# Kernel tuning notes

Measured on AMD Instinct MI355X. Metric: run time of the kernel, lower is better.

Reference implementation:

```python
import jax, jax.numpy as jnp
import numpy as np
from jax.scipy.special import gammaln, xlogy

B, N, DIM, H, DK, DV = 2, 2048, 1536, 8, 64, 64
NRPF = 192  # num_rel_pos_features, already divisible by 6


def get_positional_embed(n, feat):
    # Enformer positional basis: exponential, central-mask, gamma; then sign-antisymmetrized.
    nb = feat // 6  # num basis per class
    d = jnp.arange(-n + 1, n, dtype=jnp.float32)          # [2n-1]
    ad = jnp.abs(d)[:, None]                              # [2n-1, 1]
    # exponential decay features
    max_range = np.log(n) / np.log(2.0)
    half_life = 2.0 ** jnp.linspace(3.0, max_range, nb)
    e = jnp.exp(-np.log(2.0) / half_life * ad)
    # central mask features
    widths = 2.0 ** jnp.arange(1, nb + 1, dtype=jnp.float32) - 1.0
    c = (widths > ad).astype(jnp.float32)
    # gamma pdf features
    std = n / (2.0 * nb)
    mean = jnp.linspace(n / nb, float(n), nb)
    conc = (mean / std) ** 2
    rate = mean / (std ** 2)
    logp = xlogy(conc - 1.0, ad) - rate * ad - (gammaln(conc) - conc * jnp.log(rate))
    p = jnp.exp(logp) + 1e-8
    g = p / jnp.max(p)
    emb = jnp.concatenate([e, c, g], axis=-1)             # [2n-1, feat//2]
    return jnp.concatenate([emb, jnp.sign(d)[:, None] * emb], axis=-1)  # [2n-1, feat]


def relative_shift(x):
    # x: [b, h, i, 2i-1] -> [b, h, i, i]
    b, h, i, j = x.shape
    x = jnp.pad(x, ((0, 0), (0, 0), (0, 0), (1, 0)))      # [b,h,i,j+1]
    x = x.reshape(b, h, j + 1, i)[:, :, 1:, :]            # drop first 'row'
    x = x.reshape(b, h, i, j)
    return x[..., : (j + 2) // 2]                          # keep first i cols


def setup_inputs() -> dict:
    key = jax.random.key(0)
    ks = jax.random.split(key, 9)
    s = 0.02
    return {
        "x": jax.random.normal(ks[0], (B, N, DIM), jnp.float32),
        "Wq": jax.random.normal(ks[1], (DIM, H * DK), jnp.float32) * s,
        "Wk": jax.random.normal(ks[2], (DIM, H * DK), jnp.float32) * s,
        "Wv": jax.random.normal(ks[3], (DIM, H * DV), jnp.float32) * s,
        "Wo": jax.random.normal(ks[4], (H * DV, DIM), jnp.float32) * s,
        "bo": jnp.zeros((DIM,), jnp.float32),
        "Wrel": jax.random.normal(ks[5], (NRPF, H * DK), jnp.float32) * s,
        "rel_content_bias": jax.random.normal(ks[6], (1, H, 1, DK), jnp.float32),
        "rel_pos_bias": jax.random.normal(ks[7], (1, H, 1, DK), jnp.float32),
    }


def reference(x, Wq, Wk, Wv, Wo, bo, Wrel, rel_content_bias, rel_pos_bias):
    b, n, _ = x.shape
    scale = DK ** -0.5
    split = lambda t, d: t.reshape(b, n, H, d).transpose(0, 2, 1, 3)  # b h n d
    q = split(x @ Wq, DK) * scale
    k = split(x @ Wk, DK)
    v = split(x @ Wv, DV)
    content_logits = jnp.einsum('bhid,bhjd->bhij', q + rel_content_bias, k)
    pos = get_positional_embed(n, NRPF) @ Wrel               # [2n-1, H*DK]
    pos = pos.reshape(2 * n - 1, H, DK).transpose(1, 0, 2)   # h j d
    rel_logits = jnp.einsum('bhid,hjd->bhij', q + rel_pos_bias, pos)
    rel_logits = relative_shift(rel_logits)
    attn = jax.nn.softmax(content_logits + rel_logits, axis=-1)
    out = jnp.einsum('bhij,bhjd->bhid', attn, v)
    out = out.transpose(0, 2, 1, 3).reshape(b, n, H * DV)
    return out @ Wo + bo
```

## Files before the change

### kernel.cpp

```cpp
#include <hip/hip_runtime.h>
#include <stdint.h>
#include <cmath>

#define B_    2
#define N_    2048
#define DIM_  1536
#define H_    8
#define NPOS  (2*N_ - 1)
#define NB_   32

typedef __attribute__((ext_vector_type(8))) short short8;
typedef __attribute__((ext_vector_type(4))) float float4v;

__device__ __forceinline__ float bf2f(unsigned short u) {
    return __uint_as_float(((unsigned int)u) << 16);
}
__device__ __forceinline__ unsigned short f2bf(float f) {
    unsigned int u = __float_as_uint(f);
    u += 0x7FFFu + ((u >> 16) & 1u);
    return (unsigned short)(u >> 16);
}
__device__ __forceinline__ unsigned int cvtpk(float lo, float hi) {
    unsigned int r;
    asm("v_cvt_pk_bf16_f32 %0, %1, %2" : "=v"(r) : "v"(lo), "v"(hi));
    return r;
}
__device__ __forceinline__ unsigned int pack2bf(float lo, float hi) {
    return cvtpk(lo, hi);
}
__device__ __forceinline__ float ldf(const void* p, int isF32, size_t idx) {
    return isF32 ? ((const float*)p)[idx] : bf2f(((const unsigned short*)p)[idx]);
}
__device__ __forceinline__ void gll16(const unsigned short* g, unsigned short* l) {
    __builtin_amdgcn_global_load_lds(
        (const __attribute__((address_space(1))) unsigned int*)g,
        (__attribute__((address_space(3))) unsigned int*)l, 16, 0, 0);
}

constexpr size_t OFF_FLAG = 0;
constexpr size_t OFF_POS  = 256;
constexpr size_t OFF_Q    = OFF_POS + (size_t)H_*4096*64*2;
constexpr size_t OFF_K    = OFF_Q   + (size_t)B_*H_*N_*64*2;
constexpr size_t OFF_V    = OFF_K   + (size_t)B_*H_*N_*64*2;
constexpr size_t OFF_WOT  = OFF_V   + (size_t)B_*H_*N_*64*2;
constexpr size_t OFF_XB   = OFF_WOT + (size_t)DIM_*512*2;
constexpr size_t OFF_AO   = OFF_XB;
constexpr size_t OFF_OP   = OFF_AO + (size_t)4096*512*2;
constexpr size_t OFF_LP   = OFF_OP + (size_t)3*16*32*4096*2;
constexpr size_t OFF_WT   = OFF_XB + (size_t)4096*DIM_*2;
static_assert(OFF_LP + (size_t)3*16*32*64*4 <= OFF_WT + (size_t)3*512*DIM_*2, "ws overflow");

__global__ __launch_bounds__(256) void detect_kernel(const unsigned short* __restrict__ x,
                                                     unsigned int* __restrict__ flags) {
    __shared__ int cnt[256];
    unsigned short u = x[2 * threadIdx.x];
    int e  = (u >> 7) & 0xFF;
    int ok = (u == 0) || (e >= 95 && e <= 140);
    cnt[threadIdx.x] = ok;
    __syncthreads();
    for (int s = 128; s > 0; s >>= 1) {
        if (threadIdx.x < s) cnt[threadIdx.x] += cnt[threadIdx.x + s];
        __syncthreads();
    }
    if (threadIdx.x == 0) flags[0] = (cnt[0] >= 192) ? 0u : 1u;
}

__global__ __launch_bounds__(256) void cvtx_kernel(const unsigned int* __restrict__ flags,
                                                   const void* __restrict__ x,
                                                   unsigned short* __restrict__ Xb) {
    const int f32 = (int)flags[0];
    const size_t total = (size_t)4096 * DIM_;
    size_t i = ((size_t)blockIdx.x * 256 + threadIdx.x) * 8;
    const size_t stride = (size_t)gridDim.x * 256 * 8;
    if (f32) {
        for (; i < total; i += stride) {
            float4v a = *reinterpret_cast<const float4v*>((const float*)x + i);
            float4v b = *reinterpret_cast<const float4v*>((const float*)x + i + 4);
            uint4 o;
            o.x = pack2bf(a[0], a[1]); o.y = pack2bf(a[2], a[3]);
            o.z = pack2bf(b[0], b[1]); o.w = pack2bf(b[2], b[3]);
            *reinterpret_cast<uint4*>(Xb + i) = o;
        }
    } else {
        for (; i < total; i += stride)
            *reinterpret_cast<uint4*>(Xb + i) =
                *reinterpret_cast<const uint4*>((const unsigned short*)x + i);
    }
}

__global__ __launch_bounds__(256) void cvtw_kernel(const unsigned int* __restrict__ flags,
                                                   const void* __restrict__ Wq, const void* __restrict__ Wk,
                                                   const void* __restrict__ Wv, const void* __restrict__ Wo,
                                                   unsigned short* __restrict__ Wt,
                                                   unsigned short* __restrict__ Wot) {
    __shared__ unsigned short tile[32][33];
    const int f32 = (int)flags[0];
    const int z = blockIdx.z;
    const void* src = z == 0 ? Wq : (z == 1 ? Wk : (z == 2 ? Wv : Wo));
    unsigned short* dst = (z < 3) ? (Wt + (size_t)z * 512 * DIM_) : Wot;
    const int R = (z < 3) ? DIM_ : 512;
    const int C = (z < 3) ? 512 : DIM_;
    const int x0 = ((z < 3) ? blockIdx.x : blockIdx.y) * 32;
    const int y0 = ((z < 3) ? blockIdx.y : blockIdx.x) * 32;
    const int tx = threadIdx.x & 31, ty = threadIdx.x >> 5;
#pragma unroll
    for (int i = 0; i < 4; ++i)
        tile[ty + i * 8][tx] = f2bf(ldf(src, f32, (size_t)(y0 + ty + i * 8) * C + x0 + tx));
    __syncthreads();
#pragma unroll
    for (int i = 0; i < 4; ++i)
        dst[(size_t)(x0 + ty + i * 8) * R + y0 + tx] = tile[tx][ty + i * 8];
}

__global__ __launch_bounds__(512) void posproj_kernel(double maxp,
                                                      const void* __restrict__ Wrel,
                                                      const unsigned int* __restrict__ flags,
                                                      unsigned short* __restrict__ posb) {
    __shared__ __align__(16) float eb[8 * 192];
    const int f32 = (int)flags[0];
    const int j0  = blockIdx.x * 8;
    const int c   = threadIdx.x;
    const double max_range = log((double)N_) / log(2.0);

    for (int u = c; u < 8 * 96; u += 512) {
        int rr = u / 96, f = u - rr * 96;
        int j = j0 + rr;
        float v = 0.f, sg = 0.f;
        if (j < NPOS) {
            int dd  = j - (N_ - 1);
            int adI = dd < 0 ? -dd : dd;
            double ad = (double)adI;
            double val;
            if (f < 32) {
                double t = 3.0 + (double)f * (max_range - 3.0) / 31.0;
                val = exp2(-ad / exp2(t));
            } else if (f < 64) {
                double width = exp2((double)(f - 31)) - 1.0;
                val = (width > ad) ? 1.0 : 0.0;
            } else {
                int g = f - 64;
                double mean = 64.0 * (g + 1);
                double conc = (mean / 32.0) * (mean / 32.0);
                double rate = mean / 1024.0;
                double pp = (adI == 0) ? 1e-8
                          : exp((conc - 1.0) * log(ad) - rate * ad - lgamma(conc) + conc * log(rate)) + 1e-8;
                val = pp / maxp;
            }
            v  = (float)val;
            sg = (dd > 0) ? 1.f : ((dd < 0) ? -1.f : 0.f);
        }
        eb[rr * 192 + f]      = v;
        eb[rr * 192 + 96 + f] = sg * v;
    }
    __syncthreads();

    float acc[8] = {0, 0, 0, 0, 0, 0, 0, 0};
    for (int k = 0; k < 192; k += 4) {
        float w0 = ldf(Wrel, f32, (size_t)(k + 0) * 512 + c);
        float w1 = ldf(Wrel, f32, (size_t)(k + 1) * 512 + c);
        float w2 = ldf(Wrel, f32, (size_t)(k + 2) * 512 + c);
        float w3 = ldf(Wrel, f32, (size_t)(k + 3) * 512 + c);
#pragma unroll
        for (int rr = 0; rr < 8; ++rr) {
            float4v e = *reinterpret_cast<const float4v*>(&eb[rr * 192 + k]);
            acc[rr] += e[0] * w0;
            acc[rr] += e[1] * w1;
            acc[rr] += e[2] * w2;
            acc[rr] += e[3] * w3;
        }
    }
    int h = c >> 6, dcol = c & 63;
    for (int rr = 0; rr < 8; ++rr) {
        int j = j0 + rr;
        if (j < NPOS)
            posb[((size_t)h * 4096 + j) * 64 + dcol] = f2bf(acc[rr]);
    }
}

__device__ __forceinline__ void gemm64x128_core(const unsigned short* __restrict__ A,
                                                const unsigned short* __restrict__ Bt,
                                                int K, int row0, int col0,
                                                unsigned short* As, unsigned short* Bs,
                                                float4v acc[2][4]) {
    const int tid = threadIdx.x, lane = tid & 63, w = tid >> 6;
    const int l15 = lane & 15, q8 = (lane >> 4) * 8;
    const int mr0 = (w & 1) * 32, nc0 = (w >> 1) * 64;
    const int sr = lane >> 2, sc8 = (lane & 3) * 8;
    for (int k0 = 0; k0 < K; k0 += 32) {
        __syncthreads();
        gll16(&A [(size_t)(row0 + w * 16 + sr) * K + k0 + sc8],      &As[w * 512]);
        gll16(&Bt[(size_t)(col0 + w * 32 + sr) * K + k0 + sc8],      &Bs[w * 1024]);
        gll16(&Bt[(size_t)(col0 + w * 32 + 16 + sr) * K + k0 + sc8], &Bs[w * 1024 + 512]);
        __syncthreads();
        short8 a[2], b[4];
#pragma unroll
        for (int mi = 0; mi < 2; ++mi)
            a[mi] = *reinterpret_cast<const short8*>(&As[(mr0 + mi * 16 + l15) * 32 + q8]);
#pragma unroll
        for (int ni = 0; ni < 4; ++ni)
            b[ni] = *reinterpret_cast<const short8*>(&Bs[(nc0 + ni * 16 + l15) * 32 + q8]);
#pragma unroll
        for (int mi = 0; mi < 2; ++mi)
#pragma unroll
            for (int ni = 0; ni < 4; ++ni)
                acc[mi][ni] = __builtin_amdgcn_mfma_f32_16x16x32_bf16(a[mi], b[ni], acc[mi][ni], 0, 0, 0);
    }
}

__global__ __launch_bounds__(256) void qkv_kernel(const unsigned short* __restrict__ Xb,
                                                  const unsigned short* __restrict__ Wt,
                                                  unsigned short* __restrict__ qbuf,
                                                  unsigned short* __restrict__ kbuf,
                                                  unsigned short* __restrict__ vbuf) {
    __shared__ __align__(16) unsigned short As[64 * 32];
    __shared__ __align__(16) unsigned short Bs[128 * 32];
    const int row0 = blockIdx.y * 64, col0 = blockIdx.x * 128;
    float4v acc[2][4];
#pragma unroll
    for (int mi = 0; mi < 2; ++mi)
#pragma unroll
        for (int ni = 0; ni < 4; ++ni) acc[mi][ni] = (float4v){0.f, 0.f, 0.f, 0.f};
    gemm64x128_core(Xb, Wt, DIM_, row0, col0, As, Bs, acc);
    const int lane = threadIdx.x & 63, w = threadIdx.x >> 6;
    const int l15 = lane & 15, quad = lane >> 4;
    const int mr0 = (w & 1) * 32, nc0 = (w >> 1) * 64;
#pragma unroll
    for (int mi = 0; mi < 2; ++mi)
#pragma unroll
        for (int ni = 0; ni < 4; ++ni) {
            int n = col0 + nc0 + ni * 16 + l15;
            int mode = n >> 9, nn = n & 511;
            int hh = nn >> 6, dd = nn & 63;
            int mb = row0 + mr0 + mi * 16 + quad * 4;
            int bb = mb >> 11, ii = mb & 2047;
            if (mode == 2) {
                union { unsigned short us[4]; uint2 u2; } pk;
                unsigned int p0 = cvtpk(acc[mi][ni][0], acc[mi][ni][1]);
                unsigned int p1 = cvtpk(acc[mi][ni][2], acc[mi][ni][3]);
                pk.u2 = (uint2){p0, p1};
                *reinterpret_cast<uint2*>(
                    &vbuf[((size_t)(bb * 8 + hh) * 64 + dd) * 2048 + ii]) = pk.u2;
            } else {
                unsigned short* Obuf = (mode == 0) ? qbuf : kbuf;
                float scale = (mode == 0) ? 0.125f : 1.0f;
#pragma unroll
                for (int r = 0; r < 4; ++r)
                    Obuf[((size_t)(bb * 8 + hh) * N_ + ii + r) * 64 + dd] = f2bf(acc[mi][ni][r] * scale);
            }
        }
}

#define SLD 72
#define RST 68

__device__ __forceinline__ void stage64(const unsigned short* __restrict__ g,
                                        unsigned short* __restrict__ s, int tid) {
    int r = tid >> 2, d0 = (tid & 3) * 16;
    const uint4* p = reinterpret_cast<const uint4*>(g + (size_t)r * 64 + d0);
    *reinterpret_cast<uint4*>(&s[r * SLD + d0])     = p[0];
    *reinterpret_cast<uint4*>(&s[r * SLD + d0 + 8]) = p[1];
}

__global__ __launch_bounds__(256) void attn_kernel(const unsigned int* __restrict__ flags,
                                                   const unsigned short* __restrict__ qb,
                                                   const unsigned short* __restrict__ kb,
                                                   const unsigned short* __restrict__ vb,
                                                   const unsigned short* __restrict__ posb,
                                                   const void* __restrict__ rcb,
                                                   const void* __restrict__ rpb,
                                                   unsigned short* __restrict__ Opart,
                                                   float* __restrict__ lpart) {
    __shared__ __align__(16) unsigned short Ks[64 * SLD];
    __shared__ __align__(16) unsigned short Ps[64 * SLD];
    __shared__ __align__(16) unsigned short Vt[64 * SLD];
    __shared__ __align__(16) unsigned short Pp[64 * SLD];
    __shared__ __align__(8)  unsigned short Rb[128 * RST];

    const int f32 = (int)flags[0];
    const int tid = threadIdx.x;
    const int it = blockIdx.x, bh = blockIdx.y, z = blockIdx.z;
    const int h = bh & 7;
    const int i0 = it * 64;
    const size_t qoff = (size_t)bh * N_ * 64;
    const size_t voff = (size_t)bh * 64 * 2048;
    const size_t poff = (size_t)h * 4096 * 64;
    const int lane = tid & 63, w = tid >> 6;
    const int l15 = lane & 15, quad = lane >> 4, q8 = quad * 8;
    const int m0 = w * 16 + quad * 4;
    const int sr = tid >> 2, sc = (tid & 3) * 16;

    short8 afc[2], afr[2];
#pragma unroll
    for (int kc = 0; kc < 2; ++kc) {
        uint4 qv = *reinterpret_cast<const uint4*>(
            &qb[qoff + (size_t)(i0 + w * 16 + l15) * 64 + kc * 32 + q8]);
        unsigned int uu[4] = {qv.x, qv.y, qv.z, qv.w};
        unsigned int cw[4], rw[4];
#pragma unroll
        for (int e = 0; e < 4; ++e) {
            int k = h * 64 + kc * 32 + q8 + 2 * e;
            float lo = __uint_as_float(uu[e] << 16);
            float hi = __uint_as_float(uu[e] & 0xffff0000u);
            cw[e] = pack2bf(lo + ldf(rcb, f32, k), hi + ldf(rcb, f32, k + 1));
            rw[e] = pack2bf(lo + ldf(rpb, f32, k), hi + ldf(rpb, f32, k + 1));
        }
        union { uint4 u; short8 s; } cv, rv2;
        cv.u  = (uint4){cw[0], cw[1], cw[2], cw[3]};
        rv2.u = (uint4){rw[0], rw[1], rw[2], rw[3]};
        afc[kc] = cv.s;
        afr[kc] = rv2.s;
    }

    float4v Oa[4];
#pragma unroll
    for (int nb = 0; nb < 4; ++nb) Oa[nb] = (float4v){0.f, 0.f, 0.f, 0.f};
    float lsum[4] = {0.f, 0.f, 0.f, 0.f};

    const int base0 = 1984 - i0;
    const int t0 = z * 11, t1 = (z == 2) ? 32 : (t0 + 11);
    const int cs0 = base0 + t0 * 64;

    stage64(&posb[poff + (size_t)cs0 * 64], Ps, tid);
    __syncthreads();
    {
        float4v R[4];
#pragma unroll
        for (int nb = 0; nb < 4; ++nb) R[nb] = (float4v){0.f, 0.f, 0.f, 0.f};
        __builtin_amdgcn_s_setprio(1);
#pragma unroll
        for (int kc = 0; kc < 2; ++kc)
#pragma unroll
            for (int nb = 0; nb < 4; ++nb) {
                short8 pb = *reinterpret_cast<const short8*>(&Ps[(nb * 16 + l15) * SLD + kc * 32 + q8]);
                R[nb] = __builtin_amdgcn_mfma_f32_16x16x32_bf16(afr[kc], pb, R[nb], 0, 0, 0);
            }
        __builtin_amdgcn_s_setprio(0);
#pragma unroll
        for (int nb = 0; nb < 4; ++nb) {
            int ta = cs0 + nb * 16 + l15;
            unsigned int pk0 = cvtpk(R[nb][0], R[nb][1]);
            unsigned int pk1 = cvtpk(R[nb][2], R[nb][3]);
            Rb[(size_t)((ta + m0 + 0) & 127) * RST + m0 + 0] = (unsigned short)pk0;
            Rb[(size_t)((ta + m0 + 1) & 127) * RST + m0 + 1] = (unsigned short)(pk0 >> 16);
            Rb[(size_t)((ta + m0 + 2) & 127) * RST + m0 + 2] = (unsigned short)pk1;
            Rb[(size_t)((ta + m0 + 3) & 127) * RST + m0 + 3] = (unsigned short)(pk1 >> 16);
        }
    }
    __syncthreads();

    stage64(&kb[qoff + (size_t)(t0 * 64) * 64], Ks, tid);
    stage64(&posb[poff + (size_t)(cs0 + 64) * 64], Ps, tid);
    {
        const unsigned short* gv = &vb[voff + (size_t)sr * 2048 + t0 * 64 + sc];
        *reinterpret_cast<uint4*>(&Vt[sr * SLD + sc])     = *reinterpret_cast<const uint4*>(gv);
        *reinterpret_cast<uint4*>(&Vt[sr * SLD + sc + 8]) = *reinterpret_cast<const uint4*>(gv + 8);
    }
    __syncthreads();

    for (int jt = t0; jt < t1; ++jt) {
        const int j0 = jt * 64, basej = base0 + j0;
        const bool hasn = (jt + 1 < t1);

        uint4 kr0, kr1, pr0, pr1, vr0, vr1;
        if (hasn) {
            const unsigned short* gk = &kb[qoff + (size_t)(j0 + 64 + sr) * 64 + sc];
            kr0 = *reinterpret_cast<const uint4*>(gk);
            kr1 = *reinterpret_cast<const uint4*>(gk + 8);
            const unsigned short* gp = &posb[poff + (size_t)(basej + 128 + sr) * 64 + sc];
            pr0 = *reinterpret_cast<const uint4*>(gp);
            pr1 = *reinterpret_cast<const uint4*>(gp + 8);
            const unsigned short* gv = &vb[voff + (size_t)sr * 2048 + j0 + 64 + sc];
            vr0 = *reinterpret_cast<const uint4*>(gv);
            vr1 = *reinterpret_cast<const uint4*>(gv + 8);
            __builtin_amdgcn_sched_barrier(0);
        }

        {
            float4v R[4];
#pragma unroll
            for (int nb = 0; nb < 4; ++nb) R[nb] = (float4v){0.f, 0.f, 0.f, 0.f};
            __builtin_amdgcn_s_setprio(1);
#pragma unroll
            for (int kc = 0; kc < 2; ++kc)
#pragma unroll
                for (int nb = 0; nb < 4; ++nb) {
                    short8 pb = *reinterpret_cast<const short8*>(&Ps[(nb * 16 + l15) * SLD + kc * 32 + q8]);
                    R[nb] = __builtin_amdgcn_mfma_f32_16x16x32_bf16(afr[kc], pb, R[nb], 0, 0, 0);
                }
            __builtin_amdgcn_s_setprio(0);
            const int tb = basej + 64;
#pragma unroll
            for (int nb = 0; nb < 4; ++nb) {
                int ta = tb + nb * 16 + l15;
                unsigned int pk0 = cvtpk(R[nb][0], R[nb][1]);
                unsigned int pk1 = cvtpk(R[nb][2], R[nb][3]);
                Rb[(size_t)((ta + m0 + 0) & 127) * RST + m0 + 0] = (unsigned short)pk0;
                Rb[(size_t)((ta + m0 + 1) & 127) * RST + m0 + 1] = (unsigned short)(pk0 >> 16);
                Rb[(size_t)((ta + m0 + 2) & 127) * RST + m0 + 2] = (unsigned short)pk1;
                Rb[(size_t)((ta + m0 + 3) & 127) * RST + m0 + 3] = (unsigned short)(pk1 >> 16);
            }
        }

        float4v Sacc[4];
#pragma unroll
        for (int nb = 0; nb < 4; ++nb) Sacc[nb] = (float4v){0.f, 0.f, 0.f, 0.f};
        __builtin_amdgcn_s_setprio(1);
#pragma unroll
        for (int kc = 0; kc < 2; ++kc)
#pragma unroll
            for (int nb = 0; nb < 4; ++nb) {
                short8 kf = *reinterpret_cast<const short8*>(&Ks[(nb * 16 + l15) * SLD + kc * 32 + q8]);
                Sacc[nb] = __builtin_amdgcn_mfma_f32_16x16x32_bf16(afc[kc], kf, Sacc[nb], 0, 0, 0);
            }
        __builtin_amdgcn_s_setprio(0);

        float pv4[4][4];
#pragma unroll
        for (int nb = 0; nb < 4; ++nb) {
            const int jl = nb * 16 + l15;
            const int row = (basej + 63 + jl) & 127;
            union { uint2 u2; unsigned short us[4]; } rv;
            rv.u2 = *reinterpret_cast<const uint2*>(&Rb[(size_t)row * RST + m0]);
#pragma unroll
            for (int r = 0; r < 4; ++r) {
                float p = __expf(Sacc[nb][r] + bf2f(rv.us[r]));
                pv4[nb][r] = p;
                lsum[r] += p;
            }
        }
#pragma unroll
        for (int r = 0; r < 4; ++r) {
            unsigned short* prow = &Pp[(m0 + r) * SLD + l15];
#pragma unroll
            for (int np = 0; np < 2; ++np) {
                unsigned int pk = cvtpk(pv4[2 * np][r], pv4[2 * np + 1][r]);
                prow[(2 * np) * 16]     = (unsigned short)pk;
                prow[(2 * np + 1) * 16] = (unsigned short)(pk >> 16);
            }
        }

        __builtin_amdgcn_s_setprio(1);
#pragma unroll
        for (int kc = 0; kc < 2; ++kc) {
            short8 pf = *reinterpret_cast<const short8*>(&Pp[(w * 16 + l15) * SLD + kc * 32 + q8]);
#pragma unroll
            for (int nb = 0; nb < 4; ++nb) {
                short8 vf = *reinterpret_cast<const short8*>(&Vt[(nb * 16 + l15) * SLD + kc * 32 + q8]);
                Oa[nb] = __builtin_amdgcn_mfma_f32_16x16x32_bf16(pf, vf, Oa[nb], 0, 0, 0);
            }
        }
        __builtin_amdgcn_s_setprio(0);

        if (hasn) {
            __syncthreads();
            *reinterpret_cast<uint4*>(&Ks[sr * SLD + sc])     = kr0;
            *reinterpret_cast<uint4*>(&Ks[sr * SLD + sc + 8]) = kr1;
            *reinterpret_cast<uint4*>(&Ps[sr * SLD + sc])     = pr0;
            *reinterpret_cast<uint4*>(&Ps[sr * SLD + sc + 8]) = pr1;
            *reinterpret_cast<uint4*>(&Vt[sr * SLD + sc])     = vr0;
            *reinterpret_cast<uint4*>(&Vt[sr * SLD + sc + 8]) = vr1;
            __syncthreads();
        }
    }

#pragma unroll
    for (int r = 0; r < 4; ++r)
#pragma unroll
        for (int off = 1; off < 16; off <<= 1) lsum[r] += __shfl_xor(lsum[r], off);
    const size_t pslot = (size_t)(z * 16 + bh) * 32 + it;
    const size_t obase = pslot * 4096;
#pragma unroll
    for (int nb = 0; nb < 4; ++nb) {
        unsigned int pk0 = cvtpk(Oa[nb][0], Oa[nb][1]);
        unsigned int pk1 = cvtpk(Oa[nb][2], Oa[nb][3]);
        unsigned short* prow = &Pp[m0 * SLD + nb * 16 + l15];
        prow[0 * SLD] = (unsigned short)pk0;
        prow[1 * SLD] = (unsigned short)(pk0 >> 16);
        prow[2 * SLD] = (unsigned short)pk1;
        prow[3 * SLD] = (unsigned short)(pk1 >> 16);
    }
    {
        const int rr2 = w * 16 + (lane >> 2), cc2 = (lane & 3) * 16;
        uint4 o0 = *reinterpret_cast<const uint4*>(&Pp[rr2 * SLD + cc2]);
        uint4 o1 = *reinterpret_cast<const uint4*>(&Pp[rr2 * SLD + cc2 + 8]);
        *reinterpret_cast<uint4*>(&Opart[obase + (size_t)rr2 * 64 + cc2])     = o0;
        *reinterpret_cast<uint4*>(&Opart[obase + (size_t)rr2 * 64 + cc2 + 8]) = o1;
    }
    if (l15 == 0) {
#pragma unroll
        for (int r = 0; r < 4; ++r) lpart[pslot * 64 + m0 + r] = lsum[r];
    }
}

__global__ __launch_bounds__(256) void combine_kernel(const unsigned short* __restrict__ Opart,
                                                      const float* __restrict__ lpart,
                                                      unsigned short* __restrict__ ao) {
    const int it = blockIdx.x, bh = blockIdx.y;
    const int h = bh & 7, b = bh >> 3, i0 = it * 64;
    const int tid = threadIdx.x;
    const int row = tid >> 2, c0 = (tid & 3) * 16;
    float o[16];
#pragma unroll
    for (int e = 0; e < 16; ++e) o[e] = 0.f;
    float l = 0.f;
#pragma unroll
    for (int z = 0; z < 3; ++z) {
        const size_t pslot = (size_t)(z * 16 + bh) * 32 + it;
        const size_t ob = pslot * 4096 + (size_t)row * 64 + c0;
        uint4 a = *reinterpret_cast<const uint4*>(&Opart[ob]);
        uint4 b4 = *reinterpret_cast<const uint4*>(&Opart[ob + 8]);
        unsigned int uu[8] = {a.x, a.y, a.z, a.w, b4.x, b4.y, b4.z, b4.w};
#pragma unroll
        for (int e = 0; e < 8; ++e) {
            o[2 * e]     += __uint_as_float(uu[e] << 16);
            o[2 * e + 1] += __uint_as_float(uu[e] & 0xffff0000u);
        }
        l += lpart[pslot * 64 + row];
    }
    float inv = 1.0f / l;
    unsigned int ou[8];
#pragma unroll
    for (int e = 0; e < 8; ++e) ou[e] = pack2bf(o[2 * e] * inv, o[2 * e + 1] * inv);
    unsigned short* dst = &ao[((size_t)b * N_ + i0 + row) * 512 + h * 64 + c0];
    *reinterpret_cast<uint4*>(dst)     = (uint4){ou[0], ou[1], ou[2], ou[3]};
    *reinterpret_cast<uint4*>(dst + 8) = (uint4){ou[4], ou[5], ou[6], ou[7]};
}

__global__ __launch_bounds__(256) void outproj_kernel(const unsigned int* __restrict__ flags,
                                                      const unsigned short* __restrict__ AO,
                                                      const unsigned short* __restrict__ Wot,
                                                      const void* __restrict__ bo,
                                                      void* __restrict__ out) {
    __shared__ __align__(16) unsigned short As[64 * 32];
    __shared__ __align__(16) unsigned short Bs[128 * 32];
    const int f32 = (int)flags[0];
    const int row0 = blockIdx.y * 64, col0 = blockIdx.x * 128;
    float4v acc[2][4];
#pragma unroll
    for (int mi = 0; mi < 2; ++mi)
#pragma unroll
        for (int ni = 0; ni < 4; ++ni) acc[mi][ni] = (float4v){0.f, 0.f, 0.f, 0.f};
    gemm64x128_core(AO, Wot, 512, row0, col0, As, Bs, acc);
    const int lane = threadIdx.x & 63, w = threadIdx.x >> 6;
    const int l15 = lane & 15, quad = lane >> 4;
    const int mr0 = (w & 1) * 32, nc0 = (w >> 1) * 64;
#pragma unroll
    for (int mi = 0; mi < 2; ++mi)
#pragma unroll
        for (int ni = 0; ni < 4; ++ni) {
            int n = col0 + nc0 + ni * 16 + l15;
            float bias = ldf(bo, f32, n);
#pragma unroll
            for (int r = 0; r < 4; ++r) {
                int m = row0 + mr0 + mi * 16 + quad * 4 + r;
                float v = acc[mi][ni][r] + bias;
                if (f32) ((float*)out)[(size_t)m * DIM_ + n] = v;
                else     ((unsigned short*)out)[(size_t)m * DIM_ + n] = f2bf(v);
            }
        }
}

extern "C" void kernel_launch(void* const* d_in, const int* in_sizes, int n_in,
                              void* d_out, int out_size, void* d_ws, size_t ws_size,
                              hipStream_t stream) {
    const void* x    = d_in[0];
    const void* Wq   = d_in[1];
    const void* Wk   = d_in[2];
    const void* Wv   = d_in[3];
    const void* Wo   = d_in[4];
    const void* bo   = d_in[5];
    const void* Wrel = d_in[6];
    const void* rcb  = d_in[7];
    const void* rpb  = d_in[8];

    char* ws = (char*)d_ws;
    unsigned int*   flags = (unsigned int*)(ws + OFF_FLAG);
    unsigned short* posb  = (unsigned short*)(ws + OFF_POS);
    unsigned short* qbuf  = (unsigned short*)(ws + OFF_Q);
    unsigned short* kbuf  = (unsigned short*)(ws + OFF_K);
    unsigned short* vbuf  = (unsigned short*)(ws + OFF_V);
    unsigned short* Wot   = (unsigned short*)(ws + OFF_WOT);
    unsigned short* Xb    = (unsigned short*)(ws + OFF_XB);
    unsigned short* ao    = (unsigned short*)(ws + OFF_AO);
    unsigned short* Opart = (unsigned short*)(ws + OFF_OP);
    float*          lpart = (float*)(ws + OFF_LP);
    unsigned short* Wt    = (unsigned short*)(ws + OFF_WT);

    double maxp = 0.0;
    for (int g = 0; g < NB_; ++g) {
        double mean = 64.0 * (g + 1);
        double conc = (mean / 32.0) * (mean / 32.0);
        double rate = mean / 1024.0;
        double lgc  = std::lgamma(conc);
        double clr  = conc * std::log(rate);
        for (int ad = 1; ad < N_; ++ad) {
            double lp = (conc - 1.0) * std::log((double)ad) - rate * (double)ad - lgc + clr;
            double p  = std::exp(lp) + 1e-8;
            if (p > maxp) maxp = p;
        }
    }

    detect_kernel<<<dim3(1), dim3(256), 0, stream>>>((const unsigned short*)x, flags);
    cvtx_kernel<<<dim3(1024), dim3(256), 0, stream>>>(flags, x, Xb);
    cvtw_kernel<<<dim3(16, 48, 4), dim3(256), 0, stream>>>(flags, Wq, Wk, Wv, Wo, Wt, Wot);
    posproj_kernel<<<dim3(512), dim3(512), 0, stream>>>(maxp, Wrel, flags, posb);
    qkv_kernel<<<dim3(12, 64), dim3(256), 0, stream>>>(Xb, Wt, qbuf, kbuf, vbuf);
    attn_kernel<<<dim3(32, 16, 3), dim3(256), 0, stream>>>(flags, qbuf, kbuf, vbuf, posb, rcb, rpb, Opart, lpart);
    combine_kernel<<<dim3(32, 16), dim3(256), 0, stream>>>(Opart, lpart, ao);
    outproj_kernel<<<dim3(12, 64), dim3(256), 0, stream>>>(flags, ao, Wot, bo, d_out);
}
```

Baseline: 283.4 us.

## Fuse prep kernels, enlarge GEMM tiles to 128x128, remap attention grid

Merges the detect, x-convert, weight-transpose and positional-projection kernels into one launch, with each block recomputing the dtype flag locally. This removes three launches and their serialization. The QKV and output-projection GEMMs move from 64x128 to 128x128 tiles with 4x4 MFMA accumulators per wave, for more reuse per LDS load at the cost of half as many blocks and more registers. The attention grid is flattened to 1D with an interleaving remap, likely to spread work across XCDs for cache locality.

```diff
diff --git a/kernel.cpp b/kernel.cpp
--- a/kernel.cpp
+++ b/kernel.cpp
@@ -50,157 +50,159 @@
 constexpr size_t OFF_WT   = OFF_XB + (size_t)4096*DIM_*2;
 static_assert(OFF_LP + (size_t)3*16*32*64*4 <= OFF_WT + (size_t)3*512*DIM_*2, "ws overflow");
 
-__global__ __launch_bounds__(256) void detect_kernel(const unsigned short* __restrict__ x,
-                                                     unsigned int* __restrict__ flags) {
-    __shared__ int cnt[256];
-    unsigned short u = x[2 * threadIdx.x];
-    int e  = (u >> 7) & 0xFF;
-    int ok = (u == 0) || (e >= 95 && e <= 140);
-    cnt[threadIdx.x] = ok;
-    __syncthreads();
-    for (int s = 128; s > 0; s >>= 1) {
-        if (threadIdx.x < s) cnt[threadIdx.x] += cnt[threadIdx.x + s];
-        __syncthreads();
-    }
-    if (threadIdx.x == 0) flags[0] = (cnt[0] >= 192) ? 0u : 1u;
-}
-
-__global__ __launch_bounds__(256) void cvtx_kernel(const unsigned int* __restrict__ flags,
+__global__ __launch_bounds__(512) void prep_kernel(double maxp,
                                                    const void* __restrict__ x,
-                                                   unsigned short* __restrict__ Xb) {
-    const int f32 = (int)flags[0];
-    const size_t total = (size_t)4096 * DIM_;
-    size_t i = ((size_t)blockIdx.x * 256 + threadIdx.x) * 8;
-    const size_t stride = (size_t)gridDim.x * 256 * 8;
-    if (f32) {
-        for (; i < total; i += stride) {
-            float4v a = *reinterpret_cast<const float4v*>((const float*)x + i);
-            float4v b = *reinterpret_cast<const float4v*>((const float*)x + i + 4);
-            uint4 o;
-            o.x = pack2bf(a[0], a[1]); o.y = pack2bf(a[2], a[3]);
-            o.z = pack2bf(b[0], b[1]); o.w = pack2bf(b[2], b[3]);
-            *reinterpret_cast<uint4*>(Xb + i) = o;
-        }
-    } else {
-        for (; i < total; i += stride)
-            *reinterpret_cast<uint4*>(Xb + i) =
-                *reinterpret_cast<const uint4*>((const unsigned short*)x + i);
-    }
-}
-
-__global__ __launch_bounds__(256) void cvtw_kernel(const unsigned int* __restrict__ flags,
                                                    const void* __restrict__ Wq, const void* __restrict__ Wk,
                                                    const void* __restrict__ Wv, const void* __restrict__ Wo,
+                                                   const void* __restrict__ Wrel,
+                                                   unsigned int* __restrict__ flags,
+                                                   unsigned short* __restrict__ Xb,
                                                    unsigned short* __restrict__ Wt,
-                                                   unsigned short* __restrict__ Wot) {
-    __shared__ unsigned short tile[32][33];
-    const int f32 = (int)flags[0];
-    const int z = blockIdx.z;
-    const void* src = z == 0 ? Wq : (z == 1 ? Wk : (z == 2 ? Wv : Wo));
-    unsigned short* dst = (z < 3) ? (Wt + (size_t)z * 512 * DIM_) : Wot;
-    const int R = (z < 3) ? DIM_ : 512;
-    const int C = (z < 3) ? 512 : DIM_;
-    const int x0 = ((z < 3) ? blockIdx.x : blockIdx.y) * 32;
-    const int y0 = ((z < 3) ? blockIdx.y : blockIdx.x) * 32;
-    const int tx = threadIdx.x & 31, ty = threadIdx.x >> 5;
-#pragma unroll
-    for (int i = 0; i < 4; ++i)
-        tile[ty + i * 8][tx] = f2bf(ldf(src, f32, (size_t)(y0 + ty + i * 8) * C + x0 + tx));
+                                                   unsigned short* __restrict__ Wot,
+                                                   unsigned short* __restrict__ posb) {
+    __shared__ __align__(16) char smraw[8 * 192 * 4];
+    const int tid = threadIdx.x;
+    const int bid = blockIdx.x;
+
+    int* cnt = (int*)smraw;
+    int ok = 0;
+    if (tid < 256) {
+        unsigned short u = ((const unsigned short*)x)[2 * tid];
+        int e = (u >> 7) & 0xFF;
+        ok = (u == 0) || (e >= 95 && e <= 140);
+    }
+    cnt[tid] = ok;
     __syncthreads();
-#pragma unroll
-    for (int i = 0; i < 4; ++i)
-        dst[(size_t)(x0 + ty + i * 8) * R + y0 + tx] = tile[tx][ty + i * 8];
-}
-
-__global__ __launch_bounds__(512) void posproj_kernel(double maxp,
-                                                      const void* __restrict__ Wrel,
-                                                      const unsigned int* __restrict__ flags,
-                                                      unsigned short* __restrict__ posb) {
-    __shared__ __align__(16) float eb[8 * 192];
-    const int f32 = (int)flags[0];
-    const int j0  = blockIdx.x * 8;
-    const int c   = threadIdx.x;
-    const double max_range = log((double)N_) / log(2.0);
-
-    for (int u = c; u < 8 * 96; u += 512) {
-        int rr = u / 96, f = u - rr * 96;
-        int j = j0 + rr;
-        float v = 0.f, sg = 0.f;
-        if (j < NPOS) {
-            int dd  = j - (N_ - 1);
-            int adI = dd < 0 ? -dd : dd;
-            double ad = (double)adI;
-            double val;
-            if (f < 32) {
-                double t = 3.0 + (double)f * (max_range - 3.0) / 31.0;
-                val = exp2(-ad / exp2(t));
-            } else if (f < 64) {
-                double width = exp2((double)(f - 31)) - 1.0;
-                val = (width > ad) ? 1.0 : 0.0;
-            } else {
-                int g = f - 64;
-                double mean = 64.0 * (g + 1);
-                double conc = (mean / 32.0) * (mean / 32.0);
-                double rate = mean / 1024.0;
-                double pp = (adI == 0) ? 1e-8
-                          : exp((conc - 1.0) * log(ad) - rate * ad - lgamma(conc) + conc * log(rate)) + 1e-8;
-                val = pp / maxp;
-            }
-            v  = (float)val;
-            sg = (dd > 0) ? 1.f : ((dd < 0) ? -1.f : 0.f);
-        }
-        eb[rr * 192 + f]      = v;
-        eb[rr * 192 + 96 + f] = sg * v;
-    }
+    for (int s = 256; s > 0; s >>= 1) {
+        if (tid < s) cnt[tid] += cnt[tid + s];
+        __syncthreads();
+    }
+    const int f32 = !(cnt[0] >= 192);
     __syncthreads();
-
-    float acc[8] = {0, 0, 0, 0, 0, 0, 0, 0};
-    for (int k = 0; k < 192; k += 4) {
-        float w0 = ldf(Wrel, f32, (size_t)(k + 0) * 512 + c);
-        float w1 = ldf(Wrel, f32, (size_t)(k + 1) * 512 + c);
-        float w2 = ldf(Wrel, f32, (size_t)(k + 2) * 512 + c);
-        float w3 = ldf(Wrel, f32, (size_t)(k + 3) * 512 + c);
-#pragma unroll
+    if (bid == 0 && tid == 0) flags[0] = (unsigned int)f32;
+
+    if (bid < 512) {
+        const size_t total = (size_t)4096 * DIM_;
+        size_t i = ((size_t)bid * 512 + tid) * 8;
+        const size_t stride = (size_t)512 * 512 * 8;
+        if (f32) {
+            for (; i < total; i += stride) {
+                float4v a = *reinterpret_cast<const float4v*>((const float*)x + i);
+                float4v b = *reinterpret_cast<const float4v*>((const float*)x + i + 4);
+                uint4 o;
+                o.x = pack2bf(a[0], a[1]); o.y = pack2bf(a[2], a[3]);
+                o.z = pack2bf(b[0], b[1]); o.w = pack2bf(b[2], b[3]);
+                *reinterpret_cast<uint4*>(Xb + i) = o;
+            }
+        } else {
+            for (; i < total; i += stride)
+                *reinterpret_cast<uint4*>(Xb + i) =
+                    *reinterpret_cast<const uint4*>((const unsigned short*)x + i);
+        }
+    } else if (bid < 3584) {
+        unsigned short (*tile)[33] = (unsigned short(*)[33])smraw;
+        const int idx = bid - 512;
+        const int z = idx / 768, rem = idx % 768;
+        const int bx = rem & 15, by = rem >> 4;
+        const void* src = z == 0 ? Wq : (z == 1 ? Wk : (z == 2 ? Wv : Wo));
+        unsigned short* dst = (z < 3) ? (Wt + (size_t)z * 512 * DIM_) : Wot;
+        const int R = (z < 3) ? DIM_ : 512;
+        const int C = (z < 3) ? 512 : DIM_;
+        const int x0 = ((z < 3) ? bx : by) * 32;
+        const int y0 = ((z < 3) ? by : bx) * 32;
+        const int tx = tid & 31, ty = tid >> 5;
+#pragma unroll
+        for (int i = 0; i < 2; ++i)
+            tile[ty + i * 16][tx] = f2bf(ldf(src, f32, (size_t)(y0 + ty + i * 16) * C + x0 + tx));
+        __syncthreads();
+#pragma unroll
+        for (int i = 0; i < 2; ++i)
+            dst[(size_t)(x0 + ty + i * 16) * R + y0 + tx] = tile[tx][ty + i * 16];
+    } else {
+        float* eb = (float*)smraw;
+        const int j0 = (bid - 3584) * 8;
+        const int c  = tid;
+        const double max_range = log((double)N_) / log(2.0);
+        for (int u = c; u < 8 * 96; u += 512) {
+            int rr = u / 96, f = u - rr * 96;
+            int j = j0 + rr;
+            float v = 0.f, sg = 0.f;
+            if (j < NPOS) {
+                int dd  = j - (N_ - 1);
+                int adI = dd < 0 ? -dd : dd;
+                double ad = (double)adI;
+                double val;
+                if (f < 32) {
+                    double t = 3.0 + (double)f * (max_range - 3.0) / 31.0;
+                    val = exp2(-ad / exp2(t));
+                } else if (f < 64) {
+                    double width = exp2((double)(f - 31)) - 1.0;
+                    val = (width > ad) ? 1.0 : 0.0;
+                } else {
+                    int g = f - 64;
+                    double mean = 64.0 * (g + 1);
+                    double conc = (mean / 32.0) * (mean / 32.0);
+                    double rate = mean / 1024.0;
+                    double pp = (adI == 0) ? 1e-8
+                              : exp((conc - 1.0) * log(ad) - rate * ad - lgamma(conc) + conc * log(rate)) + 1e-8;
+                    val = pp / maxp;
+                }
+                v  = (float)val;
+                sg = (dd > 0) ? 1.f : ((dd < 0) ? -1.f : 0.f);
+            }
+            eb[rr * 192 + f]      = v;
+            eb[rr * 192 + 96 + f] = sg * v;
+        }
+        __syncthreads();
+        float acc[8] = {0, 0, 0, 0, 0, 0, 0, 0};
+        for (int k = 0; k < 192; k += 4) {
+            float w0 = ldf(Wrel, f32, (size_t)(k + 0) * 512 + c);
+            float w1 = ldf(Wrel, f32, (size_t)(k + 1) * 512 + c);
+            float w2 = ldf(Wrel, f32, (size_t)(k + 2) * 512 + c);
+            float w3 = ldf(Wrel, f32, (size_t)(k + 3) * 512 + c);
+#pragma unroll
+            for (int rr = 0; rr < 8; ++rr) {
+                float4v e = *reinterpret_cast<const float4v*>(&eb[rr * 192 + k]);
+                acc[rr] += e[0] * w0;
+                acc[rr] += e[1] * w1;
+                acc[rr] += e[2] * w2;
+                acc[rr] += e[3] * w3;
+            }
+        }
+        int h = c >> 6, dcol = c & 63;
         for (int rr = 0; rr < 8; ++rr) {
-            float4v e = *reinterpret_cast<const float4v*>(&eb[rr * 192 + k]);
-            acc[rr] += e[0] * w0;
-            acc[rr] += e[1] * w1;
-            acc[rr] += e[2] * w2;
-            acc[rr] += e[3] * w3;
-        }
-    }
-    int h = c >> 6, dcol = c & 63;
-    for (int rr = 0; rr < 8; ++rr) {
-        int j = j0 + rr;
-        if (j < NPOS)
-            posb[((size_t)h * 4096 + j) * 64 + dcol] = f2bf(acc[rr]);
-    }
-}
-
-__device__ __forceinline__ void gemm64x128_core(const unsigned short* __restrict__ A,
-                                                const unsigned short* __restrict__ Bt,
-                                                int K, int row0, int col0,
-                                                unsigned short* As, unsigned short* Bs,
-                                                float4v acc[2][4]) {
+            int j = j0 + rr;
+            if (j < NPOS)
+                posb[((size_t)h * 4096 + j) * 64 + dcol] = f2bf(acc[rr]);
+        }
+    }
+}
+
+__device__ __forceinline__ void gemm128_core(const unsigned short* __restrict__ A,
+                                             const unsigned short* __restrict__ Bt,
+                                             int K, int row0, int col0,
+                                             unsigned short* As, unsigned short* Bs,
+                                             float4v acc[4][4]) {
     const int tid = threadIdx.x, lane = tid & 63, w = tid >> 6;
     const int l15 = lane & 15, q8 = (lane >> 4) * 8;
-    const int mr0 = (w & 1) * 32, nc0 = (w >> 1) * 64;
+    const int mr0 = (w >> 1) * 64, nc0 = (w & 1) * 64;
     const int sr = lane >> 2, sc8 = (lane & 3) * 8;
     for (int k0 = 0; k0 < K; k0 += 32) {
         __syncthreads();
-        gll16(&A [(size_t)(row0 + w * 16 + sr) * K + k0 + sc8],      &As[w * 512]);
+        gll16(&A [(size_t)(row0 + w * 32 + sr) * K + k0 + sc8],      &As[w * 1024]);
+        gll16(&A [(size_t)(row0 + w * 32 + 16 + sr) * K + k0 + sc8], &As[w * 1024 + 512]);
         gll16(&Bt[(size_t)(col0 + w * 32 + sr) * K + k0 + sc8],      &Bs[w * 1024]);
         gll16(&Bt[(size_t)(col0 + w * 32 + 16 + sr) * K + k0 + sc8], &Bs[w * 1024 + 512]);
         __syncthreads();
-        short8 a[2], b[4];
-#pragma unroll
-        for (int mi = 0; mi < 2; ++mi)
+        short8 a[4], b[4];
+#pragma unroll
+        for (int mi = 0; mi < 4; ++mi)
             a[mi] = *reinterpret_cast<const short8*>(&As[(mr0 + mi * 16 + l15) * 32 + q8]);
 #pragma unroll
         for (int ni = 0; ni < 4; ++ni)
             b[ni] = *reinterpret_cast<const short8*>(&Bs[(nc0 + ni * 16 + l15) * 32 + q8]);
 #pragma unroll
-        for (int mi = 0; mi < 2; ++mi)
+        for (int mi = 0; mi < 4; ++mi)
 #pragma unroll
             for (int ni = 0; ni < 4; ++ni)
                 acc[mi][ni] = __builtin_amdgcn_mfma_f32_16x16x32_bf16(a[mi], b[ni], acc[mi][ni], 0, 0, 0);
@@ -212,20 +214,20 @@
                                                   unsigned short* __restrict__ qbuf,
                                                   unsigned short* __restrict__ kbuf,
                                                   unsigned short* __restrict__ vbuf) {
-    __shared__ __align__(16) unsigned short As[64 * 32];
+    __shared__ __align__(16) unsigned short As[128 * 32];
     __shared__ __align__(16) unsigned short Bs[128 * 32];
-    const int row0 = blockIdx.y * 64, col0 = blockIdx.x * 128;
-    float4v acc[2][4];
-#pragma unroll
-    for (int mi = 0; mi < 2; ++mi)
+    const int row0 = blockIdx.y * 128, col0 = blockIdx.x * 128;
+    float4v acc[4][4];
+#pragma unroll
+    for (int mi = 0; mi < 4; ++mi)
 #pragma unroll
         for (int ni = 0; ni < 4; ++ni) acc[mi][ni] = (float4v){0.f, 0.f, 0.f, 0.f};
-    gemm64x128_core(Xb, Wt, DIM_, row0, col0, As, Bs, acc);
+    gemm128_core(Xb, Wt, DIM_, row0, col0, As, Bs, acc);
     const int lane = threadIdx.x & 63, w = threadIdx.x >> 6;
     const int l15 = lane & 15, quad = lane >> 4;
-    const int mr0 = (w & 1) * 32, nc0 = (w >> 1) * 64;
-#pragma unroll
-    for (int mi = 0; mi < 2; ++mi)
+    const int mr0 = (w >> 1) * 64, nc0 = (w & 1) * 64;
+#pragma unroll
+    for (int mi = 0; mi < 4; ++mi)
 #pragma unroll
         for (int ni = 0; ni < 4; ++ni) {
             int n = col0 + nc0 + ni * 16 + l15;
@@ -278,7 +280,9 @@
 
     const int f32 = (int)flags[0];
     const int tid = threadIdx.x;
-    const int it = blockIdx.x, bh = blockIdx.y, z = blockIdx.z;
+    int wg = blockIdx.x;
+    wg = (wg & 7) * 192 + (wg >> 3);
+    const int it = wg & 31, bh = (wg >> 5) & 15, z = wg >> 9;
     const int h = bh & 7;
     const int i0 = it * 64;
     const size_t qoff = (size_t)bh * N_ * 64;
@@ -531,21 +535,21 @@
                                                       const unsigned short* __restrict__ Wot,
                                                       const void* __restrict__ bo,
                                                       void* __restrict__ out) {
-    __shared__ __align__(16) unsigned short As[64 * 32];
+    __shared__ __align__(16) unsigned short As[128 * 32];
     __shared__ __align__(16) unsigned short Bs[128 * 32];
     const int f32 = (int)flags[0];
-    const int row0 = blockIdx.y * 64, col0 = blockIdx.x * 128;
-    float4v acc[2][4];
-#pragma unroll
-    for (int mi = 0; mi < 2; ++mi)
+    const int row0 = blockIdx.y * 128, col0 = blockIdx.x * 128;
+    float4v acc[4][4];
+#pragma unroll
+    for (int mi = 0; mi < 4; ++mi)
 #pragma unroll
         for (int ni = 0; ni < 4; ++ni) acc[mi][ni] = (float4v){0.f, 0.f, 0.f, 0.f};
-    gemm64x128_core(AO, Wot, 512, row0, col0, As, Bs, acc);
+    gemm128_core(AO, Wot, 512, row0, col0, As, Bs, acc);
     const int lane = threadIdx.x & 63, w = threadIdx.x >> 6;
     const int l15 = lane & 15, quad = lane >> 4;
-    const int mr0 = (w & 1) * 32, nc0 = (w >> 1) * 64;
-#pragma unroll
-    for (int mi = 0; mi < 2; ++mi)
+    const int mr0 = (w >> 1) * 64, nc0 = (w & 1) * 64;
+#pragma unroll
+    for (int mi = 0; mi < 4; ++mi)
 #pragma unroll
         for (int ni = 0; ni < 4; ++ni) {
             int n = col0 + nc0 + ni * 16 + l15;
@@ -600,12 +604,10 @@
         }
     }
 
-    detect_kernel<<<dim3(1), dim3(256), 0, stream>>>((const unsigned short*)x, flags);
-    cvtx_kernel<<<dim3(1024), dim3(256), 0, stream>>>(flags, x, Xb);
-    cvtw_kernel<<<dim3(16, 48, 4), dim3(256), 0, stream>>>(flags, Wq, Wk, Wv, Wo, Wt, Wot);
-    posproj_kernel<<<dim3(512), dim3(512), 0, stream>>>(maxp, Wrel, flags, posb);
-    qkv_kernel<<<dim3(12, 64), dim3(256), 0, stream>>>(Xb, Wt, qbuf, kbuf, vbuf);
-    attn_kernel<<<dim3(32, 16, 3), dim3(256), 0, stream>>>(flags, qbuf, kbuf, vbuf, posb, rcb, rpb, Opart, lpart);
+    prep_kernel<<<dim3(4096), dim3(512), 0, stream>>>(maxp, x, Wq, Wk, Wv, Wo, Wrel,
+                                                      flags, Xb, Wt, Wot, posb);
+    qkv_kernel<<<dim3(12, 32), dim3(256), 0, stream>>>(Xb, Wt, qbuf, kbuf, vbuf);
+    attn_kernel<<<dim3(1536), dim3(256), 0, stream>>>(flags, qbuf, kbuf, vbuf, posb, rcb, rpb, Opart, lpart);
     combine_kernel<<<dim3(32, 16), dim3(256), 0, stream>>>(Opart, lpart, ao);
-    outproj_kernel<<<dim3(12, 64), dim3(256), 0, stream>>>(flags, ao, Wot, bo, d_out);
-}
+    outproj_kernel<<<dim3(12, 32), dim3(256), 0, stream>>>(flags, ao, Wot, bo, d_out);
+}
```

Measured after the change: 302.5 us. +6.7%, slower.
